# Optimization experiments

Measured on AMD Instinct MI355X. Metric: run time of the kernel, lower is better.

## Reference

```python
import jax, jax.numpy as jnp
import numpy as np

DIMS, HEAD, FREQ = 1024, 16, 10000
HEAD_DIM = DIMS // HEAD          # 64
ROT = HEAD_DIM // 2              # 32
B, S = 4, 8192


def setup_inputs() -> dict:
    key = jax.random.key(0)
    k1, k2, k3, k4 = jax.random.split(key, 4)
    x = jax.random.normal(k1, (B, S, DIMS), dtype=jnp.float32)
    matrix = jax.random.normal(k2, (HEAD_DIM, HEAD_DIM), dtype=jnp.float32)
    thetas = jax.random.normal(k3, (ROT,), dtype=jnp.float32) * 0.1
    tscale = jnp.ones((1,), dtype=jnp.float32)
    # inverse frequencies exactly as in __init__
    invf = (1.0 / FREQ ** (jnp.arange(0, HEAD_DIM, 2, dtype=jnp.float32) / HEAD_DIM)).astype(jnp.float32)
    pairs = jax.random.randint(k4, (ROT, 2), 0, HEAD_DIM, dtype=jnp.int32)
    return {"x": x, "matrix": matrix, "thetas": thetas, "tscale": tscale,
            "invf": invf, "pairs": pairs}


def _composed_rotation(thetas, tscale, pairs, d, dtype):
    # Build every Givens matrix G_k (same element-set order as the torch code)
    theta = thetas * tscale[0]

    def make_G(i, j, th):
        c, sn = jnp.cos(th), jnp.sin(th)
        G = jnp.eye(d, dtype=dtype)
        return G.at[i, i].set(c).at[j, j].set(c).at[i, j].set(-sn).at[j, i].set(sn)

    Gs = jax.vmap(make_G)(pairs[:, 0], pairs[:, 1], theta)  # [rot, d, d]

    def step(acc, G):
        return acc @ G, None

    G_comb, _ = jax.lax.scan(step, jnp.eye(d, dtype=dtype), Gs)
    return G_comb


def reference(x, matrix, thetas, tscale, invf, pairs):
    b, s, dims = x.shape
    d = matrix.shape[0]          # head_dim
    h = dims // d                # heads

    G_comb = _composed_rotation(thetas, tscale, pairs, d, x.dtype)

    xr = x.reshape(b, s, h, d)
    # flat @ G_combined @ self.matrix (acts on last dim)
    xr = xr @ (G_comb @ matrix)

    # sinusoidal RoPE: sinusoid[s, d/2] = pos * invf
    pos = jnp.arange(s, dtype=x.dtype)
    sinusoid = pos[:, None] * invf[None, :]
    sin = jnp.sin(sinusoid)[None, :, None, :]   # [1, s, 1, d/2]
    cos = jnp.cos(sinusoid)[None, :, None, :]

    x1, x2 = xr[..., ::2], xr[..., 1::2]
    out = jnp.concatenate([x1 * cos - x2 * sin, x1 * sin + x2 * cos], axis=-1)
    return out.reshape(b, s, dims) * jnp.asarray(np.sqrt(dims), x.dtype)
```

## Files before the change

### kernel.cpp

```cpp
#include <hip/hip_runtime.h>
#include <math.h>

#define BB 4
#define SS 8192
#define HH 16
#define DD 64
#define ROT 32
#define NG (BB * SS * HH)
#define RPT 64
#define TILES 4
#define NBLK (NG / (RPT * TILES))
#define TPB 256
#define LSTR 65

typedef float f32x4 __attribute__((ext_vector_type(4)));
typedef float f32x2 __attribute__((ext_vector_type(2)));
typedef short bf16x8 __attribute__((ext_vector_type(8)));

__global__ void setup_GM(const float* __restrict__ thetas,
                         const float* __restrict__ tscale,
                         const int* __restrict__ pairs,
                         const float* __restrict__ matrix,
                         float* __restrict__ M,
                         unsigned short* __restrict__ Mhi,
                         unsigned short* __restrict__ Mlo) {
  __shared__ float Gs[DD][DD];
  const int t = threadIdx.x;
  if (t < DD) {
    for (int c = 0; c < DD; ++c) Gs[t][c] = (t == c) ? 1.0f : 0.0f;
    const float ts = tscale[0];
    for (int r = 0; r < ROT; ++r) {
      const int i = pairs[2 * r], j = pairs[2 * r + 1];
      const float th = thetas[r] * ts;
      const float cc = cosf(th), sn = sinf(th);
      if (i == j) {
        Gs[t][i] *= sn;
      } else {
        const float a = Gs[t][i], b = Gs[t][j];
        Gs[t][i] = a * cc + b * sn;
        Gs[t][j] = b * cc - a * sn;
      }
    }
  }
  __syncthreads();
  const int e = blockIdx.x * 256 + t;
  const int k = e >> 6, col = e & 63;
  float a0 = 0.f, a1 = 0.f, a2 = 0.f, a3 = 0.f;
  for (int kk = 0; kk < DD; kk += 4) {
    a0 = fmaf(Gs[k][kk], matrix[kk * DD + col], a0);
    a1 = fmaf(Gs[k][kk + 1], matrix[(kk + 1) * DD + col], a1);
    a2 = fmaf(Gs[k][kk + 2], matrix[(kk + 2) * DD + col], a2);
    a3 = fmaf(Gs[k][kk + 3], matrix[(kk + 3) * DD + col], a3);
  }
  const float val = (a0 + a1) + (a2 + a3);
  M[e] = val;

  const int G = col & 3;
  const int v = col >> 2;
  const int lane = ((k >> 3) & 3) * 16 + v;
  const int f = G * 2 + (k >> 5);
  const int idx = (f * 64 + lane) * 8 + (k & 7);
  const unsigned int b = __float_as_uint(val);
  const unsigned int hb = b & 0xFFFF0000u;
  const float rem = val - __uint_as_float(hb);
  Mhi[idx] = (unsigned short)(b >> 16);
  Mlo[idx] = (unsigned short)(__float_as_uint(rem) >> 16);
}

__global__ void setup_tab2(const float* __restrict__ invf,
                           float* __restrict__ tab2) {
  const int idx = blockIdx.x * 256 + threadIdx.x;
  if (idx >= SS * 16) return;
  const int s = idx >> 4, v = idx & 15;
  const float a0 = (float)s * invf[2 * v];
  const float a1 = (float)s * invf[2 * v + 1];
  float4 t;
  t.x = 32.0f * cosf(a0);
  t.y = 32.0f * sinf(a0);
  t.z = 32.0f * cosf(a1);
  t.w = 32.0f * sinf(a1);
  ((float4*)tab2)[idx] = t;
}

__device__ __forceinline__ unsigned int pack_hi(float u, float v, float& ru,
                                                float& rv) {
  const unsigned int bu = __float_as_uint(u);
  const unsigned int bv = __float_as_uint(v);
  const unsigned int hv = bv & 0xFFFF0000u;
  ru = u - __uint_as_float(bu & 0xFFFF0000u);
  rv = v - __uint_as_float(hv);
  return (bu >> 16) | hv;
}
__device__ __forceinline__ unsigned int pack_lo(float ru, float rv) {
  return (__float_as_uint(ru) >> 16) | (__float_as_uint(rv) & 0xFFFF0000u);
}
__device__ __forceinline__ void cvt8(const f32x4 a, const f32x4 b, bf16x8& hi,
                                     bf16x8& lo) {
  unsigned int* hp = (unsigned int*)&hi;
  unsigned int* lp = (unsigned int*)&lo;
  float r0, r1;
  hp[0] = pack_hi(a[0], a[1], r0, r1);
  lp[0] = pack_lo(r0, r1);
  hp[1] = pack_hi(a[2], a[3], r0, r1);
  lp[1] = pack_lo(r0, r1);
  hp[2] = pack_hi(b[0], b[1], r0, r1);
  lp[2] = pack_lo(r0, r1);
  hp[3] = pack_hi(b[2], b[3], r0, r1);
  lp[3] = pack_lo(r0, r1);
}

__global__ __launch_bounds__(TPB, 3) void apply_rot(
    const float* __restrict__ x, const unsigned short* __restrict__ Mhi,
    const unsigned short* __restrict__ Mlo, const float* __restrict__ tab2,
    float* __restrict__ out) {
  const int tid = threadIdx.x;
  const int w = tid >> 6;
  const int l = tid & 63;
  const int l15 = l & 15, lk = l >> 4;

  bf16x8 bh[8], bl[8];
#pragma unroll
  for (int f = 0; f < 8; ++f) {
    bh[f] = *(const bf16x8*)(Mhi + (f * 64 + l) * 8);
    bl[f] = *(const bf16x8*)(Mlo + (f * 64 + l) * 8);
  }

  const size_t R0 = (size_t)blockIdx.x * (RPT * TILES);
  const float* __restrict__ xp = x + (R0 + w * 16 + l15) * DD + lk * 8;
  float* __restrict__ ob = out + (R0 + w * 16) * DD;
  const int tok0 = (int)(R0 >> 4) + w;

  f32x4 a0 = *(const f32x4*)(xp);
  f32x4 a1 = *(const f32x4*)(xp + 4);
  f32x4 a2 = *(const f32x4*)(xp + 32);
  f32x4 a3 = *(const f32x4*)(xp + 36);
  const float* __restrict__ xq = xp + (size_t)RPT * DD;
  f32x4 b0 = *(const f32x4*)(xq);
  f32x4 b1 = *(const f32x4*)(xq + 4);
  f32x4 b2 = *(const f32x4*)(xq + 32);
  f32x4 b3 = *(const f32x4*)(xq + 36);

#define PROC(C0, C1, C2, C3, T)                                               \
  {                                                                           \
    bf16x8 ah0, al0, ah1, al1;                                                \
    cvt8(C0, C1, ah0, al0);                                                   \
    cvt8(C2, C3, ah1, al1);                                                   \
    if ((T) + 2 < TILES) {           \
      const float* __restrict__ p = xp + (size_t)((T) + 2) * RPT * DD;        \
      C0 = *(const f32x4*)(p);                                                \
      C1 = *(const f32x4*)(p + 4);                                            \
      C2 = *(const f32x4*)(p + 32);                                           \
      C3 = *(const f32x4*)(p + 36);                                           \
    }                                                                         \
    const int spos = (tok0 + (T) * 4) & (SS - 1);                             \
    const f32x4 tv = *(const f32x4*)(tab2 + (size_t)spos * 64 + l15 * 4);     \
    f32x4 acc[4];                                                             \
    _Pragma("unroll") for (int G = 0; G < 4; ++G) {                           \
      f32x4 a_ = {0.f, 0.f, 0.f, 0.f};                                        \
      a_ = __builtin_amdgcn_mfma_f32_16x16x32_bf16(ah0, bh[2 * G], a_, 0, 0,  \
                                                   0);                        \
      a_ = __builtin_amdgcn_mfma_f32_16x16x32_bf16(ah1, bh[2 * G + 1], a_, 0, \
                                                   0, 0);                     \
      a_ = __builtin_amdgcn_mfma_f32_16x16x32_bf16(ah0, bl[2 * G], a_, 0, 0,  \
                                                   0);                        \
      a_ = __builtin_amdgcn_mfma_f32_16x16x32_bf16(ah1, bl[2 * G + 1], a_, 0, \
                                                   0, 0);                     \
      a_ = __builtin_amdgcn_mfma_f32_16x16x32_bf16(al0, bh[2 * G], a_, 0, 0,  \
                                                   0);                        \
      a_ = __builtin_amdgcn_mfma_f32_16x16x32_bf16(al1, bh[2 * G + 1], a_, 0, \
                                                   0, 0);                     \
      acc[G] = a_;                                                            \
    }                                                                         \
    float* __restrict__ og = ob + (size_t)(T)*RPT * DD;                       \
    const float cz0 = tv[0], sz0 = tv[1], cz1 = tv[2], sz1 = tv[3];           \
    _Pragma("unroll") for (int q = 0; q < 4; ++q) {                           \
      const float e0 = acc[0][q], o0 = acc[1][q];                             \
      const float e1 = acc[2][q], o1 = acc[3][q];                             \
      f32x2 lo, hi;                                                           \
      lo[0] = fmaf(e0, cz0, -(o0 * sz0));                                     \
      lo[1] = fmaf(e1, cz1, -(o1 * sz1));                                     \
      hi[0] = fmaf(e0, sz0, o0 * cz0);                                        \
      hi[1] = fmaf(e1, sz1, o1 * cz1);                                        \
      const int ro = (lk * 4 + q) * DD + 2 * l15;                             \
      __builtin_nontemporal_store(lo, (f32x2*)(og + ro));                     \
      __builtin_nontemporal_store(hi, (f32x2*)(og + ro + 32));                \
    }                                                                         \
  }

#pragma unroll 1
  for (int t = 0; t < TILES; t += 2) {
    PROC(a0, a1, a2, a3, t);
    PROC(b0, b1, b2, b3, t + 1);
  }
#undef PROC
}

__global__ __launch_bounds__(256, 8) void apply_rot_fb(
    const float* __restrict__ x, const float* __restrict__ M,
    const float* __restrict__ invf, float* __restrict__ out) {
  __shared__ float lds[64 * LSTR];
  const int tid = threadIdx.x;
  const size_t R0 = (size_t)blockIdx.x * 64;
  const float4* __restrict__ xg = (const float4*)x + R0 * 16;
#pragma unroll
  for (int i = 0; i < 4; ++i) {
    const int f = i * 256 + tid;
    *(float4*)&lds[(f >> 4) * LSTR + (f & 15) * 4] = xg[f];
  }
  __syncthreads();
  const int r = tid & 63;
  const int h = __builtin_amdgcn_readfirstlane(tid >> 6);
  const float* __restrict__ Mh = M + h * 16;
  const float* __restrict__ xr = &lds[r * LSTR];
  float acc[16];
#pragma unroll
  for (int c = 0; c < 16; ++c) acc[c] = 0.0f;
#pragma unroll 4
  for (int k4 = 0; k4 < 16; ++k4) {
    const float4 xv = *(const float4*)&xr[k4 * 4];
    const float* __restrict__ m0 = Mh + k4 * 4 * DD;
#pragma unroll
    for (int c = 0; c < 16; ++c) acc[c] = fmaf(xv.x, m0[c], acc[c]);
#pragma unroll
    for (int c = 0; c < 16; ++c) acc[c] = fmaf(xv.y, m0[DD + c], acc[c]);
#pragma unroll
    for (int c = 0; c < 16; ++c) acc[c] = fmaf(xv.z, m0[2 * DD + c], acc[c]);
#pragma unroll
    for (int c = 0; c < 16; ++c) acc[c] = fmaf(xv.w, m0[3 * DD + c], acc[c]);
  }
  const int g = (int)R0 + r;
  const int spos = (g >> 4) & (SS - 1);
  float cz[8], sz[8];
#pragma unroll
  for (int d = 0; d < 8; ++d) {
    const float ang = (float)spos * invf[h * 8 + d];
    cz[d] = 32.0f * cosf(ang);
    sz[d] = 32.0f * sinf(ang);
  }
  float4 lov[2], hiv[2];
#pragma unroll
  for (int q = 0; q < 2; ++q) {
#pragma unroll
    for (int d = 0; d < 4; ++d) {
      const int dd = 4 * q + d;
      const float e = acc[2 * dd], o = acc[2 * dd + 1];
      ((float*)&lov[q])[d] = e * cz[dd] - o * sz[dd];
      ((float*)&hiv[q])[d] = e * sz[dd] + o * cz[dd];
    }
  }
  __syncthreads();
  float* __restrict__ orow = &lds[r * LSTR];
  *(float4*)&orow[8 * h + 0] = lov[0];
  *(float4*)&orow[8 * h + 4] = lov[1];
  *(float4*)&orow[32 + 8 * h + 0] = hiv[0];
  *(float4*)&orow[32 + 8 * h + 4] = hiv[1];
  __syncthreads();
  float4* __restrict__ og = (float4*)out + R0 * 16;
#pragma unroll
  for (int i = 0; i < 4; ++i) {
    const int f = i * 256 + tid;
    og[f] = *(float4*)&lds[(f >> 4) * LSTR + (f & 15) * 4];
  }
}

extern "C" void kernel_launch(void* const* d_in, const int* in_sizes, int n_in,
                              void* d_out, int out_size, void* d_ws,
                              size_t ws_size, hipStream_t stream) {
  const float* x = (const float*)d_in[0];
  const float* matrix = (const float*)d_in[1];
  const float* thetas = (const float*)d_in[2];
  const float* tscale = (const float*)d_in[3];
  const float* invf = (const float*)d_in[4];
  const int* pairs = (const int*)d_in[5];
  float* out = (float*)d_out;

  float* M = (float*)d_ws;
  unsigned short* Mhi = (unsigned short*)(M + DD * DD);
  unsigned short* Mlo = Mhi + DD * DD;
  float* tab2 = (float*)(Mlo + DD * DD);
  const size_t need =
      (size_t)DD * DD * 4 + (size_t)DD * DD * 4 + (size_t)SS * 64 * 4;
  const bool have_tab = ws_size >= need;

  setup_GM<<<16, 256, 0, stream>>>(thetas, tscale, pairs, matrix, M, Mhi, Mlo);
  if (have_tab) {
    setup_tab2<<<(SS * 16) / 256, 256, 0, stream>>>(invf, tab2);
    apply_rot<<<NBLK, TPB, 0, stream>>>(x, Mhi, Mlo, tab2, out);
  } else {
    apply_rot_fb<<<NG / 64, 256, 0, stream>>>(x, M, invf, out);
  }
}
```

Before: 265.0 us.

## Process two tokens per wave with upfront loads and regular stores

Each block now handles 8 tokens instead of 16. Each wave loads both of its tokens and their cos/sin table rows up front, then processes them through a helper function, which replaces the prefetching tile loop. Nontemporal stores become ordinary stores. This doubles the grid size and drops the software pipelining to get more parallelism and simpler scheduling. In exchange, the per-block cost of loading the B matrix fragments is amortised over half as many tokens.

```diff
diff --git a/kernel.cpp b/kernel.cpp
--- a/kernel.cpp
+++ b/kernel.cpp
@@ -7,10 +7,9 @@
 #define DD 64
 #define ROT 32
 #define NG (BB * SS * HH)
-#define RPT 64
-#define TILES 4
-#define NBLK (NG / (RPT * TILES))
 #define TPB 256
+#define TILES 2
+#define NBLK (NG / (16 * 4 * TILES))
 #define LSTR 65
 
 typedef float f32x4 __attribute__((ext_vector_type(4)));
@@ -109,6 +108,41 @@
   lp[3] = pack_lo(r0, r1);
 }
 
+__device__ __forceinline__ void proc_token(
+    const f32x4 c0, const f32x4 c1, const f32x4 c2, const f32x4 c3,
+    const f32x4 tv, const bf16x8* bh, const bf16x8* bl,
+    float* __restrict__ og, const int lk, const int l15) {
+  bf16x8 ah0, al0, ah1, al1;
+  cvt8(c0, c1, ah0, al0);
+  cvt8(c2, c3, ah1, al1);
+  f32x4 acc[4];
+#pragma unroll
+  for (int G = 0; G < 4; ++G) {
+    f32x4 a_ = {0.f, 0.f, 0.f, 0.f};
+    a_ = __builtin_amdgcn_mfma_f32_16x16x32_bf16(ah0, bh[2 * G], a_, 0, 0, 0);
+    a_ = __builtin_amdgcn_mfma_f32_16x16x32_bf16(ah1, bh[2 * G + 1], a_, 0, 0, 0);
+    a_ = __builtin_amdgcn_mfma_f32_16x16x32_bf16(ah0, bl[2 * G], a_, 0, 0, 0);
+    a_ = __builtin_amdgcn_mfma_f32_16x16x32_bf16(ah1, bl[2 * G + 1], a_, 0, 0, 0);
+    a_ = __builtin_amdgcn_mfma_f32_16x16x32_bf16(al0, bh[2 * G], a_, 0, 0, 0);
+    a_ = __builtin_amdgcn_mfma_f32_16x16x32_bf16(al1, bh[2 * G + 1], a_, 0, 0, 0);
+    acc[G] = a_;
+  }
+  const float cz0 = tv[0], sz0 = tv[1], cz1 = tv[2], sz1 = tv[3];
+#pragma unroll
+  for (int q = 0; q < 4; ++q) {
+    const float e0 = acc[0][q], o0 = acc[1][q];
+    const float e1 = acc[2][q], o1 = acc[3][q];
+    f32x2 lo, hi;
+    lo[0] = fmaf(e0, cz0, -(o0 * sz0));
+    lo[1] = fmaf(e1, cz1, -(o1 * sz1));
+    hi[0] = fmaf(e0, sz0, o0 * cz0);
+    hi[1] = fmaf(e1, sz1, o1 * cz1);
+    const int ro = (lk * 4 + q) * DD + 2 * l15;
+    *(f32x2*)(og + ro) = lo;
+    *(f32x2*)(og + ro + 32) = hi;
+  }
+}
+
 __global__ __launch_bounds__(TPB, 3) void apply_rot(
     const float* __restrict__ x, const unsigned short* __restrict__ Mhi,
     const unsigned short* __restrict__ Mlo, const float* __restrict__ tab2,
@@ -125,74 +159,26 @@
     bl[f] = *(const bf16x8*)(Mlo + (f * 64 + l) * 8);
   }
 
-  const size_t R0 = (size_t)blockIdx.x * (RPT * TILES);
-  const float* __restrict__ xp = x + (R0 + w * 16 + l15) * DD + lk * 8;
-  float* __restrict__ ob = out + (R0 + w * 16) * DD;
-  const int tok0 = (int)(R0 >> 4) + w;
-
-  f32x4 a0 = *(const f32x4*)(xp);
-  f32x4 a1 = *(const f32x4*)(xp + 4);
-  f32x4 a2 = *(const f32x4*)(xp + 32);
-  f32x4 a3 = *(const f32x4*)(xp + 36);
-  const float* __restrict__ xq = xp + (size_t)RPT * DD;
-  f32x4 b0 = *(const f32x4*)(xq);
-  f32x4 b1 = *(const f32x4*)(xq + 4);
-  f32x4 b2 = *(const f32x4*)(xq + 32);
-  f32x4 b3 = *(const f32x4*)(xq + 36);
-
-#define PROC(C0, C1, C2, C3, T)                                               \
-  {                                                                           \
-    bf16x8 ah0, al0, ah1, al1;                                                \
-    cvt8(C0, C1, ah0, al0);                                                   \
-    cvt8(C2, C3, ah1, al1);                                                   \
-    if ((T) + 2 < TILES) {           \
-      const float* __restrict__ p = xp + (size_t)((T) + 2) * RPT * DD;        \
-      C0 = *(const f32x4*)(p);                                                \
-      C1 = *(const f32x4*)(p + 4);                                            \
-      C2 = *(const f32x4*)(p + 32);                                           \
-      C3 = *(const f32x4*)(p + 36);                                           \
-    }                                                                         \
-    const int spos = (tok0 + (T) * 4) & (SS - 1);                             \
-    const f32x4 tv = *(const f32x4*)(tab2 + (size_t)spos * 64 + l15 * 4);     \
-    f32x4 acc[4];                                                             \
-    _Pragma("unroll") for (int G = 0; G < 4; ++G) {                           \
-      f32x4 a_ = {0.f, 0.f, 0.f, 0.f};                                        \
-      a_ = __builtin_amdgcn_mfma_f32_16x16x32_bf16(ah0, bh[2 * G], a_, 0, 0,  \
-                                                   0);                        \
-      a_ = __builtin_amdgcn_mfma_f32_16x16x32_bf16(ah1, bh[2 * G + 1], a_, 0, \
-                                                   0, 0);                     \
-      a_ = __builtin_amdgcn_mfma_f32_16x16x32_bf16(ah0, bl[2 * G], a_, 0, 0,  \
-                                                   0);                        \
-      a_ = __builtin_amdgcn_mfma_f32_16x16x32_bf16(ah1, bl[2 * G + 1], a_, 0, \
-                                                   0, 0);                     \
-      a_ = __builtin_amdgcn_mfma_f32_16x16x32_bf16(al0, bh[2 * G], a_, 0, 0,  \
-                                                   0);                        \
-      a_ = __builtin_amdgcn_mfma_f32_16x16x32_bf16(al1, bh[2 * G + 1], a_, 0, \
-                                                   0, 0);                     \
-      acc[G] = a_;                                                            \
-    }                                                                         \
-    float* __restrict__ og = ob + (size_t)(T)*RPT * DD;                       \
-    const float cz0 = tv[0], sz0 = tv[1], cz1 = tv[2], sz1 = tv[3];           \
-    _Pragma("unroll") for (int q = 0; q < 4; ++q) {                           \
-      const float e0 = acc[0][q], o0 = acc[1][q];                             \
-      const float e1 = acc[2][q], o1 = acc[3][q];                             \
-      f32x2 lo, hi;                                                           \
-      lo[0] = fmaf(e0, cz0, -(o0 * sz0));                                     \
-      lo[1] = fmaf(e1, cz1, -(o1 * sz1));                                     \
-      hi[0] = fmaf(e0, sz0, o0 * cz0);                                        \
-      hi[1] = fmaf(e1, sz1, o1 * cz1);                                        \
-      const int ro = (lk * 4 + q) * DD + 2 * l15;                             \
-      __builtin_nontemporal_store(lo, (f32x2*)(og + ro));                     \
-      __builtin_nontemporal_store(hi, (f32x2*)(og + ro + 32));                \
-    }                                                                         \
-  }
-
-#pragma unroll 1
-  for (int t = 0; t < TILES; t += 2) {
-    PROC(a0, a1, a2, a3, t);
-    PROC(b0, b1, b2, b3, t + 1);
-  }
-#undef PROC
+  const size_t tok0 = (size_t)blockIdx.x * 8 + w;
+  const size_t tok1 = tok0 + 4;
+  const float* __restrict__ xp0 = x + (tok0 * 16 + l15) * DD + lk * 8;
+  const float* __restrict__ xp1 = x + (tok1 * 16 + l15) * DD + lk * 8;
+
+  const f32x4 a0 = *(const f32x4*)(xp0);
+  const f32x4 a1 = *(const f32x4*)(xp0 + 4);
+  const f32x4 a2 = *(const f32x4*)(xp0 + 32);
+  const f32x4 a3 = *(const f32x4*)(xp0 + 36);
+  const int sp0 = (int)(tok0 & (SS - 1));
+  const f32x4 tv0 = *(const f32x4*)(tab2 + (size_t)sp0 * 64 + l15 * 4);
+  const f32x4 b0 = *(const f32x4*)(xp1);
+  const f32x4 b1 = *(const f32x4*)(xp1 + 4);
+  const f32x4 b2 = *(const f32x4*)(xp1 + 32);
+  const f32x4 b3 = *(const f32x4*)(xp1 + 36);
+  const int sp1 = (int)(tok1 & (SS - 1));
+  const f32x4 tv1 = *(const f32x4*)(tab2 + (size_t)sp1 * 64 + l15 * 4);
+
+  proc_token(a0, a1, a2, a3, tv0, bh, bl, out + tok0 * 16 * DD, lk, l15);
+  proc_token(b0, b1, b2, b3, tv1, bh, bl, out + tok1 * 16 * DD, lk, l15);
 }
 
 __global__ __launch_bounds__(256, 8) void apply_rot_fb(
```

Measured after the change: 255.1 us. 1.04x faster.
